# Kernel optimization log

Measured on AMD Instinct MI355X. Metric: run time of the kernel, lower is better.

## Reference

```python
import jax, jax.numpy as jnp
import numpy as np

B, M, S = 4, 1024, 1024
D, H, FF = 1024, 16, 4096
NE, P = 128, 1
HD = D // H
EPS = 1e-5


def _layer_norm(x, g, b):
    mu = x.mean(-1, keepdims=True)
    var = ((x - mu) ** 2).mean(-1, keepdims=True)
    return (x - mu) * jax.lax.rsqrt(var + EPS) * g + b


def _mha(q_in, kv_in, in_w, in_b, out_w, out_b):
    # torch nn.MultiheadAttention: packed in_proj_weight [3D, D], y = x @ W.T + b
    wq, wk, wv = in_w[:D], in_w[D:2 * D], in_w[2 * D:]
    bq, bk, bv = in_b[:D], in_b[D:2 * D], in_b[2 * D:]
    q = (q_in @ wq.T + bq).reshape(q_in.shape[0], q_in.shape[1], H, HD)
    k = (kv_in @ wk.T + bk).reshape(kv_in.shape[0], kv_in.shape[1], H, HD)
    v = (kv_in @ wv.T + bv).reshape(kv_in.shape[0], kv_in.shape[1], H, HD)
    scores = jnp.einsum('bqhd,bkhd->bhqk', q, k) / jnp.sqrt(jnp.float32(HD))
    attn = jax.nn.softmax(scores, axis=-1)
    o = jnp.einsum('bhqk,bkhd->bqhd', attn, v).reshape(q_in.shape[0], q_in.shape[1], D)
    return o @ out_w.T + out_b


def _soft_moe(h, phi, exp_w, exp_b):
    # h: [b, m, FF]; phi: [FF, n, p]
    logits = jnp.einsum('bmd,dnp->bmnp', h, phi)
    dispatch = jax.nn.softmax(logits, axis=1)  # over tokens m
    b, m, n, p = logits.shape
    combine = jax.nn.softmax(logits.reshape(b, m, n * p), axis=-1).reshape(b, m, n, p)
    slots = jnp.einsum('bmd,bmnp->bnpd', h, dispatch)  # [b, n, p, FF]
    y = jnp.einsum('bnpd,ndo->bnpo', slots, exp_w) + exp_b[None, :, None, :]  # [b, n, p, D]
    return jnp.einsum('bnpo,bmnp->bmo', y, combine)


def setup_inputs() -> dict:
    key = jax.random.key(0)
    ks = jax.random.split(key, 16)
    sc = 0.02

    def rn(k, shape):
        return jax.random.normal(k, shape, jnp.float32) * sc

    return {
        'tgt': jax.random.normal(ks[0], (B, M, D), jnp.float32),
        'memory': jax.random.normal(ks[1], (B, S, D), jnp.float32),
        'sa_in_w': rn(ks[2], (3 * D, D)), 'sa_in_b': jnp.zeros((3 * D,), jnp.float32),
        'sa_out_w': rn(ks[3], (D, D)), 'sa_out_b': jnp.zeros((D,), jnp.float32),
        'ca_in_w': rn(ks[4], (3 * D, D)), 'ca_in_b': jnp.zeros((3 * D,), jnp.float32),
        'ca_out_w': rn(ks[5], (D, D)), 'ca_out_b': jnp.zeros((D,), jnp.float32),
        'norm1_g': jnp.ones((D,), jnp.float32), 'norm1_b': jnp.zeros((D,), jnp.float32),
        'norm2_g': jnp.ones((D,), jnp.float32), 'norm2_b': jnp.zeros((D,), jnp.float32),
        'norm3_g': jnp.ones((D,), jnp.float32), 'norm3_b': jnp.zeros((D,), jnp.float32),
        'lin_w': rn(ks[6], (FF, D)), 'lin_b': jnp.zeros((FF,), jnp.float32),
        'phi': rn(ks[7], (FF, NE, P)),
        'exp_w': rn(ks[8], (NE, FF, D)), 'exp_b': jnp.zeros((NE, D), jnp.float32),
    }


def reference(tgt, memory, sa_in_w, sa_in_b, sa_out_w, sa_out_b,
              ca_in_w, ca_in_b, ca_out_w, ca_out_b,
              norm1_g, norm1_b, norm2_g, norm2_b, norm3_g, norm3_b,
              lin_w, lin_b, phi, exp_w, exp_b):
    # post-norm (norm_first=False), dropout=0 (eval)
    x = tgt
    x = _layer_norm(x + _mha(x, x, sa_in_w, sa_in_b, sa_out_w, sa_out_b), norm1_g, norm1_b)
    x = _layer_norm(x + _mha(x, memory, ca_in_w, ca_in_b, ca_out_w, ca_out_b), norm2_g, norm2_b)
    h = jax.nn.relu(x @ lin_w.T + lin_b)  # [B, M, FF]
    ff = _soft_moe(h, phi, exp_w, exp_b)  # [B, M, D]
    x = _layer_norm(x + ff, norm3_g, norm3_b)
    return x
```

## Files before the change

kernel.cpp:

```cpp
#include <hip/hip_runtime.h>
#include <cstdint>
#include <cstddef>

typedef unsigned short u16;
typedef unsigned int   u32;
typedef short bf16x8 __attribute__((ext_vector_type(8)));
typedef float f32x4  __attribute__((ext_vector_type(4)));
typedef u16   u16x8  __attribute__((ext_vector_type(8)));
typedef u16   u16x4  __attribute__((ext_vector_type(4)));
typedef u16   u16x2  __attribute__((ext_vector_type(2)));

constexpr int B_  = 4;
constexpr int M_  = 1024;
constexpr int S_  = 1024;
constexpr int D_  = 1024;
constexpr int H_  = 16;
constexpr int FF_ = 4096;
constexpr int NE_ = 128;

__device__ __forceinline__ u16 f2bf(float f) {
    u32 u = __builtin_bit_cast(u32, f);
    u = (u + 0x7fffu + ((u >> 16) & 1u)) >> 16;
    return (u16)u;
}
__device__ __forceinline__ float bf2f(u16 u) {
    u32 x = ((u32)u) << 16;
    return __builtin_bit_cast(float, x);
}
__device__ __forceinline__ void gload_lds16(const u16* g, u16* l) {
    __builtin_amdgcn_global_load_lds(
        (const __attribute__((address_space(1))) u32*)g,
        (__attribute__((address_space(3))) u32*)l, 16, 0, 0);
}

template<int OUT_BF16, int RELU, int HAS_BIAS, int WRITE_HT>
__global__ __launch_bounds__(256) void gemm64_mfma(
    const u16* __restrict__ A, const u16* __restrict__ W,
    const float* __restrict__ bias, void* __restrict__ Cout,
    u16* __restrict__ HT,
    int K, int N, int lda, int ldw,
    size_t sA, size_t sW, size_t sC)
{
    __shared__ u16 As[2][64 * 32];
    __shared__ u16 Bs[2][128 * 32];
    const int tid = threadIdx.x;
    const int w = tid >> 6, l = tid & 63;
    const int fr = l & 15, g = l >> 4;
    const int bm = blockIdx.y * 64, bn = blockIdx.x * 128;
    const u16* Ab = A + (size_t)blockIdx.z * sA;
    const u16* Wb = W + (size_t)blockIdx.z * sW;

    const int qcol = ((l & 3) ^ ((l >> 3) & 3)) * 8;
    const int srow = w * 16 + (l >> 2);
    const u16* aG  = Ab + (size_t)(bm + srow) * lda + qcol;
    const u16* bG0 = Wb + (size_t)(bn + srow) * ldw + qcol;
    const u16* bG1 = bG0 + (size_t)64 * ldw;
    const int wo = w * 512;

    const int qsw = (g ^ ((fr >> 1) & 3)) * 8;

    f32x4 acc[4][2];
#pragma unroll
    for (int m = 0; m < 4; ++m)
#pragma unroll
        for (int n = 0; n < 2; ++n)
#pragma unroll
            for (int q = 0; q < 4; ++q) acc[m][n][q] = 0.f;

    for (int k0 = 0; k0 < K; k0 += 64) {
        __syncthreads();
        gload_lds16(aG,       &As[0][wo]);
        gload_lds16(bG0,      &Bs[0][wo]);
        gload_lds16(bG1,      &Bs[0][2048 + wo]);
        gload_lds16(aG  + 32, &As[1][wo]);
        gload_lds16(bG0 + 32, &Bs[1][wo]);
        gload_lds16(bG1 + 32, &Bs[1][2048 + wo]);
        aG += 64; bG0 += 64; bG1 += 64;
        __syncthreads();
#pragma unroll
        for (int h = 0; h < 2; ++h) {
            bf16x8 af[4], bf[2];
#pragma unroll
            for (int m = 0; m < 4; ++m)
                af[m] = *(const bf16x8*)&As[h][(m * 16 + fr) * 32 + qsw];
#pragma unroll
            for (int n = 0; n < 2; ++n)
                bf[n] = *(const bf16x8*)&Bs[h][(w * 32 + n * 16 + fr) * 32 + qsw];
#pragma unroll
            for (int m = 0; m < 4; ++m)
#pragma unroll
                for (int n = 0; n < 2; ++n)
                    acc[m][n] = __builtin_amdgcn_mfma_f32_16x16x32_bf16(
                        af[m], bf[n], acc[m][n], 0, 0, 0);
        }
    }

    const int row0 = bm + g * 4;
#pragma unroll
    for (int n = 0; n < 2; ++n) {
        const int col = bn + w * 32 + n * 16 + fr;
        float bv = 0.f;
        if (HAS_BIAS) bv = bias[col];
#pragma unroll
        for (int m = 0; m < 4; ++m) {
            const int rowm = row0 + m * 16;
            u16 o[4];
#pragma unroll
            for (int j = 0; j < 4; ++j) {
                float v = acc[m][n][j] + bv;
                if (RELU) v = fmaxf(v, 0.f);
                const size_t idx = (size_t)blockIdx.z * sC +
                                   (size_t)(rowm + j) * N + col;
                if (OUT_BF16) { o[j] = f2bf(v); ((u16*)Cout)[idx] = o[j]; }
                else          { ((float*)Cout)[idx] = v; }
            }
            if (WRITE_HT) {
                u16x4 pk; pk[0] = o[0]; pk[1] = o[1]; pk[2] = o[2]; pk[3] = o[3];
                *(u16x4*)&HT[(((size_t)(rowm >> 10)) * N + col) * 1024 + (rowm & 1023)] = pk;
            }
        }
    }
}

__global__ __launch_bounds__(256) void flash_attn_kernel(
    const u16* __restrict__ Q, int qs,
    const u16* __restrict__ K, int ks,
    const u16* __restrict__ V, int vs,
    u16* __restrict__ O, int Slen)
{
    __shared__ u16 Ks[2][64][72];
    __shared__ u16 Vt[2][64][72];
    __shared__ u16 Pw[4][16][72];
    const int b = blockIdx.z, hh = blockIdx.y;
    const int m0 = blockIdx.x * 64;
    const int tid = threadIdx.x;
    const int w = tid >> 6, l = tid & 63;
    const int lq = l & 15, g = l >> 4;

    bf16x8 qf[2];
    {
        const u16* qp = Q + ((size_t)b * M_ + m0 + w * 16 + lq) * qs + hh * 64;
        u16x8 v0 = *(const u16x8*)(qp + g * 8);
        u16x8 v1 = *(const u16x8*)(qp + 32 + g * 8);
        u16x8 o0, o1;
#pragma unroll
        for (int i = 0; i < 8; ++i) {
            o0[i] = f2bf(bf2f(v0[i]) * 0.125f);
            o1[i] = f2bf(bf2f(v1[i]) * 0.125f);
        }
        qf[0] = __builtin_bit_cast(bf16x8, o0);
        qf[1] = __builtin_bit_cast(bf16x8, o1);
    }

    f32x4 acc_o[4];
#pragma unroll
    for (int nb = 0; nb < 4; ++nb)
#pragma unroll
        for (int j = 0; j < 4; ++j) acc_o[nb][j] = 0.f;
    float m_run = -1e30f, l_run = 0.f;

    const int kp = tid & 31, dg = tid >> 5;
    const int krow = tid >> 2, kcg = (tid & 3) * 16;

    const int nt = Slen >> 6;
    u16x8 kv0, kv1, va, vb;

#define ATT_LOAD(T_)                                                          \
    {                                                                         \
        const u16* kpp = K + ((size_t)b * Slen + (T_) * 64 + krow) * ks + hh * 64 + kcg; \
        kv0 = *(const u16x8*)kpp;                                             \
        kv1 = *(const u16x8*)(kpp + 8);                                       \
        const u16* vp0 = V + ((size_t)b * Slen + (T_) * 64 + 2 * kp) * vs + hh * 64 + dg * 8; \
        va = *(const u16x8*)vp0;                                              \
        vb = *(const u16x8*)(vp0 + vs);                                       \
    }
#define ATT_WRITE(BUF_)                                                       \
    {                                                                         \
        *(u16x8*)&Ks[BUF_][krow][kcg]     = kv0;                              \
        *(u16x8*)&Ks[BUF_][krow][kcg + 8] = kv1;                              \
        _Pragma("unroll") for (int i = 0; i < 8; ++i) {                       \
            u16x2 pk; pk[0] = va[i]; pk[1] = vb[i];                           \
            *(u16x2*)&Vt[BUF_][dg * 8 + i][2 * kp] = pk;                      \
        }                                                                     \
    }

    ATT_LOAD(0)
    ATT_WRITE(0)
    __syncthreads();

    for (int t = 0; t < nt; ++t) {
        if (t + 1 < nt) ATT_LOAD(t + 1)
        const int cb = t & 1;

        f32x4 s4[4];
#pragma unroll
        for (int mb = 0; mb < 4; ++mb) {
            f32x4 z = {0.f, 0.f, 0.f, 0.f};
            bf16x8 a0 = *(const bf16x8*)&Ks[cb][mb * 16 + lq][g * 8];
            bf16x8 a1 = *(const bf16x8*)&Ks[cb][mb * 16 + lq][32 + g * 8];
            z = __builtin_amdgcn_mfma_f32_16x16x32_bf16(a0, qf[0], z, 0, 0, 0);
            z = __builtin_amdgcn_mfma_f32_16x16x32_bf16(a1, qf[1], z, 0, 0, 0);
            s4[mb] = z;
        }

        float pm = -1e30f;
#pragma unroll
        for (int mb = 0; mb < 4; ++mb)
#pragma unroll
            for (int j = 0; j < 4; ++j) pm = fmaxf(pm, s4[mb][j]);
        pm = fmaxf(pm, __shfl_xor(pm, 16));
        pm = fmaxf(pm, __shfl_xor(pm, 32));

        u16 pbf[4][4];
        float ls = 0.f;
        if (__all(pm - m_run <= 8.f)) {
#pragma unroll
            for (int mb = 0; mb < 4; ++mb)
#pragma unroll
                for (int j = 0; j < 4; ++j) {
                    float p = __expf(s4[mb][j] - m_run);
                    ls += p;
                    pbf[mb][j] = f2bf(p);
                }
            ls += __shfl_xor(ls, 16);
            ls += __shfl_xor(ls, 32);
            l_run += ls;
        } else {
            const float m_new = fmaxf(m_run, pm);
            const float alpha = __expf(m_run - m_new);
#pragma unroll
            for (int mb = 0; mb < 4; ++mb)
#pragma unroll
                for (int j = 0; j < 4; ++j) {
                    float p = __expf(s4[mb][j] - m_new);
                    ls += p;
                    pbf[mb][j] = f2bf(p);
                }
            ls += __shfl_xor(ls, 16);
            ls += __shfl_xor(ls, 32);
            l_run = l_run * alpha + ls;
            m_run = m_new;
            float al[4];
#pragma unroll
            for (int j = 0; j < 4; ++j) al[j] = __shfl(alpha, 4 * g + j);
#pragma unroll
            for (int nb = 0; nb < 4; ++nb)
#pragma unroll
                for (int j = 0; j < 4; ++j) acc_o[nb][j] *= al[j];
        }

#pragma unroll
        for (int mb = 0; mb < 4; ++mb) {
            u16x4 pk;
            pk[0] = pbf[mb][0]; pk[1] = pbf[mb][1];
            pk[2] = pbf[mb][2]; pk[3] = pbf[mb][3];
            *(u16x4*)&Pw[w][lq][mb * 16 + g * 4] = pk;
        }

#pragma unroll
        for (int kc = 0; kc < 2; ++kc) {
            bf16x8 pa = *(const bf16x8*)&Pw[w][lq][kc * 32 + g * 8];
#pragma unroll
            for (int nb = 0; nb < 4; ++nb) {
                bf16x8 bv = *(const bf16x8*)&Vt[cb][nb * 16 + lq][kc * 32 + g * 8];
                acc_o[nb] = __builtin_amdgcn_mfma_f32_16x16x32_bf16(pa, bv, acc_o[nb], 0, 0, 0);
            }
        }

        if (t + 1 < nt) ATT_WRITE((t + 1) & 1)
        __syncthreads();
    }
#undef ATT_LOAD
#undef ATT_WRITE

    float linv[4];
#pragma unroll
    for (int j = 0; j < 4; ++j) linv[j] = 1.f / __shfl(l_run, 4 * g + j);
#pragma unroll
    for (int nb = 0; nb < 4; ++nb)
#pragma unroll
        for (int j = 0; j < 4; ++j) {
            const size_t row = (size_t)b * M_ + m0 + w * 16 + 4 * g + j;
            O[row * D_ + hh * 64 + nb * 16 + lq] = f2bf(acc_o[nb][j] * linv[j]);
        }
}

__global__ __launch_bounds__(256) void cvt_multi_kernel(
    const float* __restrict__ s0, u16* __restrict__ d0,
    const float* __restrict__ s1, u16* __restrict__ d1,
    const float* __restrict__ s2, u16* __restrict__ d2,
    const float* __restrict__ s3, u16* __restrict__ d3,
    const float* __restrict__ s4, u16* __restrict__ d4,
    const float* __restrict__ s5, u16* __restrict__ d5,
    const float* __restrict__ s6, u16* __restrict__ d6)
{
    int blk = blockIdx.x;
    const float* s; u16* d;
    if      (blk < 2048) { s = s0; d = d0; }
    else if (blk < 4096) { s = s1; d = d1; blk -= 2048; }
    else if (blk < 5632) { s = s2; d = d2; blk -= 4096; }
    else if (blk < 6144) { s = s3; d = d3; blk -= 5632; }
    else if (blk < 7680) { s = s4; d = d4; blk -= 6144; }
    else if (blk < 8192) { s = s5; d = d5; blk -= 7680; }
    else                 { s = s6; d = d6; blk -= 8192; }
    const size_t i = ((size_t)blk * 256 + threadIdx.x) * 8;
    float4 a = *(const float4*)(s + i);
    float4 b = *(const float4*)(s + i + 4);
    u16x8 o;
    o[0] = f2bf(a.x); o[1] = f2bf(a.y); o[2] = f2bf(a.z); o[3] = f2bf(a.w);
    o[4] = f2bf(b.x); o[5] = f2bf(b.y); o[6] = f2bf(b.z); o[7] = f2bf(b.w);
    *(u16x8*)(d + i) = o;
}

__global__ __launch_bounds__(256) void transpose_f32_bf16_kernel(
    const float* __restrict__ src, u16* __restrict__ dst, int R, int C,
    size_t sI, size_t sO)
{
    __shared__ u16 t[32][33];
    src += (size_t)blockIdx.z * sI;
    dst += (size_t)blockIdx.z * sO;
    const int c0 = blockIdx.x * 32, r0 = blockIdx.y * 32;
    const int x = threadIdx.x & 31, y = threadIdx.x >> 5;
    for (int i = y; i < 32; i += 8)
        t[i][x] = f2bf(src[(size_t)(r0 + i) * C + c0 + x]);
    __syncthreads();
    for (int i = y; i < 32; i += 8)
        dst[(size_t)(c0 + i) * R + r0 + x] = t[x][i];
}

__global__ __launch_bounds__(256) void resid_ln_kernel(
    const float* __restrict__ X, const float* __restrict__ R,
    const float* __restrict__ g, const float* __restrict__ bt,
    float* __restrict__ Y, u16* __restrict__ Ybf)
{
    __shared__ float s1[4], s2[4];
    const size_t row = blockIdx.x;
    const int tid = threadIdx.x;
    const float4 x4 = *(const float4*)(X + row * 1024 + tid * 4);
    const float4 r4 = *(const float4*)(R + row * 1024 + tid * 4);
    float v[4] = {x4.x + r4.x, x4.y + r4.y, x4.z + r4.z, x4.w + r4.w};
    float s = v[0] + v[1] + v[2] + v[3];
    float q = v[0] * v[0] + v[1] * v[1] + v[2] * v[2] + v[3] * v[3];
#pragma unroll
    for (int off = 32; off; off >>= 1) {
        s += __shfl_xor(s, off);
        q += __shfl_xor(q, off);
    }
    if ((tid & 63) == 0) { s1[tid >> 6] = s; s2[tid >> 6] = q; }
    __syncthreads();
    s = s1[0] + s1[1] + s1[2] + s1[3];
    q = s2[0] + s2[1] + s2[2] + s2[3];
    const float mu = s * (1.f / 1024.f);
    const float var = q * (1.f / 1024.f) - mu * mu;
    const float rinv = rsqrtf(var + 1e-5f);
    const float4 g4 = *(const float4*)(g + tid * 4);
    const float4 b4 = *(const float4*)(bt + tid * 4);
    float o[4];
    o[0] = (v[0] - mu) * rinv * g4.x + b4.x;
    o[1] = (v[1] - mu) * rinv * g4.y + b4.y;
    o[2] = (v[2] - mu) * rinv * g4.z + b4.z;
    o[3] = (v[3] - mu) * rinv * g4.w + b4.w;
    *(float4*)(Y + row * 1024 + tid * 4) = *(float4*)o;
    if (Ybf) {
        u16x4 ob;
        ob[0] = f2bf(o[0]); ob[1] = f2bf(o[1]);
        ob[2] = f2bf(o[2]); ob[3] = f2bf(o[3]);
        *(u16x4*)(Ybf + row * 1024 + tid * 4) = ob;
    }
}

__global__ __launch_bounds__(256) void dispatch_softmax_T_kernel(
    const float* __restrict__ logitsP, u16* __restrict__ dispT)
{
    __shared__ float red[4];
    constexpr size_t CH = (size_t)B_ * M_ * NE_;
    const int n = blockIdx.x, b = blockIdx.y;
    u16* O = dispT + ((size_t)b * NE_ + n) * M_;
    const int tid = threadIdx.x;
    float v[4];
#pragma unroll
    for (int i = 0; i < 4; ++i) {
        const size_t idx = (size_t)(b * M_ + tid + 256 * i) * NE_ + n;
        v[i] = logitsP[idx] + logitsP[CH + idx] + logitsP[2 * CH + idx] + logitsP[3 * CH + idx];
    }
    float mx = fmaxf(fmaxf(v[0], v[1]), fmaxf(v[2], v[3]));
#pragma unroll
    for (int off = 32; off; off >>= 1) mx = fmaxf(mx, __shfl_xor(mx, off));
    if ((tid & 63) == 0) red[tid >> 6] = mx;
    __syncthreads();
    mx = fmaxf(fmaxf(red[0], red[1]), fmaxf(red[2], red[3]));
    __syncthreads();
    float e[4], s = 0.f;
#pragma unroll
    for (int i = 0; i < 4; ++i) { e[i] = __expf(v[i] - mx); s += e[i]; }
#pragma unroll
    for (int off = 32; off; off >>= 1) s += __shfl_xor(s, off);
    if ((tid & 63) == 0) red[tid >> 6] = s;
    __syncthreads();
    s = red[0] + red[1] + red[2] + red[3];
    const float inv = 1.f / s;
#pragma unroll
    for (int i = 0; i < 4; ++i) O[tid + 256 * i] = f2bf(e[i] * inv);
}

__global__ __launch_bounds__(64) void combine_softmax_kernel(
    const float* __restrict__ logitsP, u16* __restrict__ comb)
{
    constexpr size_t CH = (size_t)B_ * M_ * NE_;
    const size_t row = blockIdx.x;
    const int lane = threadIdx.x;
    const size_t i0 = row * NE_ + lane;
    const size_t i1 = i0 + 64;
    float a = logitsP[i0] + logitsP[CH + i0] + logitsP[2 * CH + i0] + logitsP[3 * CH + i0];
    float c = logitsP[i1] + logitsP[CH + i1] + logitsP[2 * CH + i1] + logitsP[3 * CH + i1];
    float mx = fmaxf(a, c);
#pragma unroll
    for (int off = 32; off; off >>= 1) mx = fmaxf(mx, __shfl_xor(mx, off));
    float e0 = __expf(a - mx), e1 = __expf(c - mx);
    float s = e0 + e1;
#pragma unroll
    for (int off = 32; off; off >>= 1) s += __shfl_xor(s, off);
    const float inv = 1.f / s;
    comb[row * NE_ + lane]      = f2bf(e0 * inv);
    comb[row * NE_ + lane + 64] = f2bf(e1 * inv);
}

__global__ __launch_bounds__(256) void expert_partial_kernel(
    const float* __restrict__ slots, const float* __restrict__ exp_w,
    float* __restrict__ part)
{
    __shared__ float sl[4][512];
    const int n = blockIdx.x;
    const int c = blockIdx.y;
    const int f0 = c * 512;
    const int t = threadIdx.x;
    for (int i = t; i < 2048; i += 256) {
        const int b = i >> 9, f = i & 511;
        sl[b][f] = slots[((size_t)b * NE_ + n) * FF_ + f0 + f];
    }
    __syncthreads();
    const int d4 = t * 4;
    const float* wp = exp_w + ((size_t)n * FF_ + f0) * D_ + d4;
    f32x4 acc[4];
#pragma unroll
    for (int b = 0; b < 4; ++b)
#pragma unroll
        for (int j = 0; j < 4; ++j) acc[b][j] = 0.f;
#pragma unroll 4
    for (int f = 0; f < 512; ++f) {
        const float4 w4 = *(const float4*)wp;
        wp += D_;
#pragma unroll
        for (int b = 0; b < 4; ++b) {
            const float s = sl[b][f];
            acc[b][0] = fmaf(s, w4.x, acc[b][0]);
            acc[b][1] = fmaf(s, w4.y, acc[b][1]);
            acc[b][2] = fmaf(s, w4.z, acc[b][2]);
            acc[b][3] = fmaf(s, w4.w, acc[b][3]);
        }
    }
#pragma unroll
    for (int b = 0; b < 4; ++b)
        *(f32x4*)&part[(((size_t)c * 4 + b) * NE_ + n) * D_ + d4] = acc[b];
}

__global__ __launch_bounds__(256) void reduce_yT_kernel(
    const float* __restrict__ part, const float* __restrict__ exp_b,
    u16* __restrict__ yT)
{
    __shared__ float tile[32][33];
    const int d0 = blockIdx.x * 32, n0 = blockIdx.y * 32, b = blockIdx.z;
    const int x = threadIdx.x & 31, y = threadIdx.x >> 5;
    for (int i = y; i < 32; i += 8) {
        const int n = n0 + i;
        float s = exp_b[(size_t)n * D_ + d0 + x];
#pragma unroll
        for (int c = 0; c < 8; ++c)
            s += part[(((size_t)c * 4 + b) * NE_ + n) * D_ + d0 + x];
        tile[i][x] = s;
    }
    __syncthreads();
    for (int i = y; i < 32; i += 8)
        yT[((size_t)b * D_ + d0 + i) * NE_ + n0 + x] = f2bf(tile[x][i]);
}

extern "C" void kernel_launch(void* const* d_in, const int* in_sizes, int n_in,
                              void* d_out, int out_size, void* d_ws, size_t ws_size,
                              hipStream_t stream)
{
    const float* tgt      = (const float*)d_in[0];
    const float* memry    = (const float*)d_in[1];
    const float* sa_in_w  = (const float*)d_in[2];
    const float* sa_in_b  = (const float*)d_in[3];
    const float* sa_out_w = (const float*)d_in[4];
    const float* sa_out_b = (const float*)d_in[5];
    const float* ca_in_w  = (const float*)d_in[6];
    const float* ca_in_b  = (const float*)d_in[7];
    const float* ca_out_w = (const float*)d_in[8];
    const float* ca_out_b = (const float*)d_in[9];
    const float* norm1_g  = (const float*)d_in[10];
    const float* norm1_b  = (const float*)d_in[11];
    const float* norm2_g  = (const float*)d_in[12];
    const float* norm2_b  = (const float*)d_in[13];
    const float* norm3_g  = (const float*)d_in[14];
    const float* norm3_b  = (const float*)d_in[15];
    const float* lin_w    = (const float*)d_in[16];
    const float* lin_b    = (const float*)d_in[17];
    const float* phi      = (const float*)d_in[18];
    const float* exp_w    = (const float*)d_in[19];
    const float* exp_b    = (const float*)d_in[20];

    float* ws = (float*)d_ws;
    u16*   qkv_bf  = (u16*)(ws);
    float* proj    = ws + 6291456;
    float* x1      = ws + 10485760;
    float* x2      = ws + 14680064;
    float* logitsP = ws + 18874368;
    float* part    = ws + 20971520;
    u16*   h_bf    = (u16*)(ws + 25165824);
    u16*   hT_bf   = (u16*)(ws + 33554432);
    u16*   obuf_bf = (u16*)(ws + 41943040);
    u16*   x1_bf   = (u16*)(ws + 44040192);
    u16*   x2_bf   = (u16*)(ws + 46137344);
    u16*   tgt_bf  = (u16*)(ws + 48234496);
    u16*   mem_bf  = (u16*)(ws + 50331648);
    u16*   dispT   = (u16*)(ws + 52428800);
    u16*   comb_bf = (u16*)(ws + 52690944);
    u16*   yT_bf   = (u16*)(ws + 52953088);
    float* slots   = ws + 53215232;
    u16*   w_sa_in = (u16*)(ws + 55312384);
    u16*   w_sa_out= (u16*)(ws + 56885248);
    u16*   w_ca_in = (u16*)(ws + 57409536);
    u16*   w_ca_out= (u16*)(ws + 58982400);
    u16*   w_lin   = (u16*)(ws + 59506688);
    u16*   phiT    = (u16*)(ws + 61603840);

    constexpr size_t CH = (size_t)B_ * M_ * NE_;

    cvt_multi_kernel<<<10240, 256, 0, stream>>>(
        tgt, tgt_bf, memry, mem_bf, sa_in_w, w_sa_in, sa_out_w, w_sa_out,
        ca_in_w, w_ca_in, ca_out_w, w_ca_out, lin_w, w_lin);
    transpose_f32_bf16_kernel<<<dim3(4, 128, 1), 256, 0, stream>>>(phi, phiT, 4096, 128, 0, 0);

    gemm64_mfma<1, 0, 1, 0><<<dim3(24, 64, 1), 256, 0, stream>>>(
        tgt_bf, w_sa_in, sa_in_b, qkv_bf, nullptr, 1024, 3072, 1024, 1024, 0, 0, 0);
    flash_attn_kernel<<<dim3(16, 16, 4), 256, 0, stream>>>(
        qkv_bf, 3072, qkv_bf + 1024, 3072, qkv_bf + 2048, 3072, obuf_bf, S_);
    gemm64_mfma<0, 0, 1, 0><<<dim3(8, 64, 1), 256, 0, stream>>>(
        obuf_bf, w_sa_out, sa_out_b, proj, nullptr, 1024, 1024, 1024, 1024, 0, 0, 0);
    resid_ln_kernel<<<4096, 256, 0, stream>>>(tgt, proj, norm1_g, norm1_b, x1, x1_bf);

    u16* qca_bf = qkv_bf;
    u16* kvca_bf = qkv_bf + (size_t)4096 * 1024;
    gemm64_mfma<1, 0, 1, 0><<<dim3(8, 64, 1), 256, 0, stream>>>(
        x1_bf, w_ca_in, ca_in_b, qca_bf, nullptr, 1024, 1024, 1024, 1024, 0, 0, 0);
    gemm64_mfma<1, 0, 1, 0><<<dim3(16, 64, 1), 256, 0, stream>>>(
        mem_bf, w_ca_in + (size_t)1024 * 1024, ca_in_b + 1024,
        kvca_bf, nullptr, 1024, 2048, 1024, 1024, 0, 0, 0);
    flash_attn_kernel<<<dim3(16, 16, 4), 256, 0, stream>>>(
        qca_bf, 1024, kvca_bf, 2048, kvca_bf + 1024, 2048, obuf_bf, S_);
    gemm64_mfma<0, 0, 1, 0><<<dim3(8, 64, 1), 256, 0, stream>>>(
        obuf_bf, w_ca_out, ca_out_b, proj, nullptr, 1024, 1024, 1024, 1024, 0, 0, 0);
    resid_ln_kernel<<<4096, 256, 0, stream>>>(x1, proj, norm2_g, norm2_b, x2, x2_bf);

    gemm64_mfma<1, 1, 1, 1><<<dim3(32, 64, 1), 256, 0, stream>>>(
        x2_bf, w_lin, lin_b, h_bf, hT_bf, 1024, 4096, 1024, 1024, 0, 0, 0);
    gemm64_mfma<0, 0, 0, 0><<<dim3(1, 64, 4), 256, 0, stream>>>(
        h_bf, phiT, nullptr, logitsP, nullptr, 1024, 128, 4096, 4096,
        1024, 1024, CH);
    dispatch_softmax_T_kernel<<<dim3(NE_, B_), 256, 0, stream>>>(logitsP, dispT);
    combine_softmax_kernel<<<dim3(B_ * M_), 64, 0, stream>>>(logitsP, comb_bf);
    gemm64_mfma<0, 0, 0, 0><<<dim3(32, 2, 4), 256, 0, stream>>>(
        dispT, hT_bf, nullptr, slots, nullptr, 1024, 4096, 1024, 1024,
        (size_t)NE_ * M_, (size_t)FF_ * M_, (size_t)NE_ * FF_);
    expert_partial_kernel<<<dim3(NE_, 8), 256, 0, stream>>>(slots, exp_w, part);
    reduce_yT_kernel<<<dim3(32, 4, 4), 256, 0, stream>>>(part, exp_b, yT_bf);
    gemm64_mfma<0, 0, 0, 0><<<dim3(8, 16, 4), 256, 0, stream>>>(
        comb_bf, yT_bf, nullptr, proj, nullptr, 128, 1024, 128, 128,
        (size_t)M_ * NE_, (size_t)D_ * NE_, (size_t)M_ * D_);
    resid_ln_kernel<<<4096, 256, 0, stream>>>(x2, proj, norm3_g, norm3_b,
                                              (float*)d_out, nullptr);
}
```

Before: 785.5 us.

## Widen flash attention blocks to 128 queries and keep residual path in bf16

Flash attention now runs 512 threads per block covering 128 query rows, so each staged K/V tile is shared by twice as many queries. Only half the threads stage V, and each thread loads one K vector. Separately, the out-projection and MoE-combine GEMMs now write bf16 instead of fp32. The residual+LayerNorm kernels read bf16 inputs and emit only bf16, except the final one, which emits fp32. This cuts global memory traffic and drops the fp32 x1/x2 buffers, at the cost of extra rounding on the residual stream and fewer attention blocks in flight.

```diff
diff --git a/kernel.cpp b/kernel.cpp
--- a/kernel.cpp
+++ b/kernel.cpp
@@ -122,7 +122,7 @@
     }
 }
 
-__global__ __launch_bounds__(256) void flash_attn_kernel(
+__global__ __launch_bounds__(512) void flash_attn_kernel(
     const u16* __restrict__ Q, int qs,
     const u16* __restrict__ K, int ks,
     const u16* __restrict__ V, int vs,
@@ -130,9 +130,9 @@
 {
     __shared__ u16 Ks[2][64][72];
     __shared__ u16 Vt[2][64][72];
-    __shared__ u16 Pw[4][16][72];
+    __shared__ u16 Pw[8][16][72];
     const int b = blockIdx.z, hh = blockIdx.y;
-    const int m0 = blockIdx.x * 64;
+    const int m0 = blockIdx.x * 128;
     const int tid = threadIdx.x;
     const int w = tid >> 6, l = tid & 63;
     const int lq = l & 15, g = l >> 4;
@@ -159,28 +159,31 @@
         for (int j = 0; j < 4; ++j) acc_o[nb][j] = 0.f;
     float m_run = -1e30f, l_run = 0.f;
 
-    const int kp = tid & 31, dg = tid >> 5;
-    const int krow = tid >> 2, kcg = (tid & 3) * 16;
+    const int krow = tid >> 3, kcg = (tid & 7) * 8;
+    const int kp = tid & 31, dg = (tid >> 5) & 7;
+    const int vstage = (tid < 256);
 
     const int nt = Slen >> 6;
-    u16x8 kv0, kv1, va, vb;
+    u16x8 kv0, va, vb;
 
 #define ATT_LOAD(T_)                                                          \
     {                                                                         \
         const u16* kpp = K + ((size_t)b * Slen + (T_) * 64 + krow) * ks + hh * 64 + kcg; \
         kv0 = *(const u16x8*)kpp;                                             \
-        kv1 = *(const u16x8*)(kpp + 8);                                       \
-        const u16* vp0 = V + ((size_t)b * Slen + (T_) * 64 + 2 * kp) * vs + hh * 64 + dg * 8; \
-        va = *(const u16x8*)vp0;                                              \
-        vb = *(const u16x8*)(vp0 + vs);                                       \
+        if (vstage) {                                                         \
+            const u16* vp0 = V + ((size_t)b * Slen + (T_) * 64 + 2 * kp) * vs + hh * 64 + dg * 8; \
+            va = *(const u16x8*)vp0;                                          \
+            vb = *(const u16x8*)(vp0 + vs);                                   \
+        }                                                                     \
     }
 #define ATT_WRITE(BUF_)                                                       \
     {                                                                         \
-        *(u16x8*)&Ks[BUF_][krow][kcg]     = kv0;                              \
-        *(u16x8*)&Ks[BUF_][krow][kcg + 8] = kv1;                              \
-        _Pragma("unroll") for (int i = 0; i < 8; ++i) {                       \
-            u16x2 pk; pk[0] = va[i]; pk[1] = vb[i];                           \
-            *(u16x2*)&Vt[BUF_][dg * 8 + i][2 * kp] = pk;                      \
+        *(u16x8*)&Ks[BUF_][krow][kcg] = kv0;                                  \
+        if (vstage) {                                                         \
+            _Pragma("unroll") for (int i = 0; i < 8; ++i) {                   \
+                u16x2 pk; pk[0] = va[i]; pk[1] = vb[i];                       \
+                *(u16x2*)&Vt[BUF_][dg * 8 + i][2 * kp] = pk;                  \
+            }                                                                 \
         }                                                                     \
     }
 
@@ -328,17 +331,28 @@
         dst[(size_t)(c0 + i) * R + r0 + x] = t[x][i];
 }
 
+template<int X_BF16, int OUT_F32>
 __global__ __launch_bounds__(256) void resid_ln_kernel(
-    const float* __restrict__ X, const float* __restrict__ R,
+    const void* __restrict__ X, const u16* __restrict__ Rb,
     const float* __restrict__ g, const float* __restrict__ bt,
-    float* __restrict__ Y, u16* __restrict__ Ybf)
+    void* __restrict__ Yout)
 {
     __shared__ float s1[4], s2[4];
     const size_t row = blockIdx.x;
     const int tid = threadIdx.x;
-    const float4 x4 = *(const float4*)(X + row * 1024 + tid * 4);
-    const float4 r4 = *(const float4*)(R + row * 1024 + tid * 4);
-    float v[4] = {x4.x + r4.x, x4.y + r4.y, x4.z + r4.z, x4.w + r4.w};
+    float xv[4];
+    if (X_BF16) {
+        u16x4 x4 = *(const u16x4*)((const u16*)X + row * 1024 + tid * 4);
+#pragma unroll
+        for (int i = 0; i < 4; ++i) xv[i] = bf2f(x4[i]);
+    } else {
+        float4 x4 = *(const float4*)((const float*)X + row * 1024 + tid * 4);
+        xv[0] = x4.x; xv[1] = x4.y; xv[2] = x4.z; xv[3] = x4.w;
+    }
+    u16x4 r4 = *(const u16x4*)(Rb + row * 1024 + tid * 4);
+    float v[4];
+#pragma unroll
+    for (int i = 0; i < 4; ++i) v[i] = xv[i] + bf2f(r4[i]);
     float s = v[0] + v[1] + v[2] + v[3];
     float q = v[0] * v[0] + v[1] * v[1] + v[2] * v[2] + v[3] * v[3];
 #pragma unroll
@@ -360,12 +374,13 @@
     o[1] = (v[1] - mu) * rinv * g4.y + b4.y;
     o[2] = (v[2] - mu) * rinv * g4.z + b4.z;
     o[3] = (v[3] - mu) * rinv * g4.w + b4.w;
-    *(float4*)(Y + row * 1024 + tid * 4) = *(float4*)o;
-    if (Ybf) {
+    if (OUT_F32) {
+        *(float4*)((float*)Yout + row * 1024 + tid * 4) = *(float4*)o;
+    } else {
         u16x4 ob;
         ob[0] = f2bf(o[0]); ob[1] = f2bf(o[1]);
         ob[2] = f2bf(o[2]); ob[3] = f2bf(o[3]);
-        *(u16x4*)(Ybf + row * 1024 + tid * 4) = ob;
+        *(u16x4*)((u16*)Yout + row * 1024 + tid * 4) = ob;
     }
 }
 
@@ -512,9 +527,7 @@
 
     float* ws = (float*)d_ws;
     u16*   qkv_bf  = (u16*)(ws);
-    float* proj    = ws + 6291456;
-    float* x1      = ws + 10485760;
-    float* x2      = ws + 14680064;
+    u16*   proj_bf = (u16*)(ws + 6291456);
     float* logitsP = ws + 18874368;
     float* part    = ws + 20971520;
     u16*   h_bf    = (u16*)(ws + 25165824);
@@ -544,11 +557,11 @@
 
     gemm64_mfma<1, 0, 1, 0><<<dim3(24, 64, 1), 256, 0, stream>>>(
         tgt_bf, w_sa_in, sa_in_b, qkv_bf, nullptr, 1024, 3072, 1024, 1024, 0, 0, 0);
-    flash_attn_kernel<<<dim3(16, 16, 4), 256, 0, stream>>>(
+    flash_attn_kernel<<<dim3(8, 16, 4), 512, 0, stream>>>(
         qkv_bf, 3072, qkv_bf + 1024, 3072, qkv_bf + 2048, 3072, obuf_bf, S_);
-    gemm64_mfma<0, 0, 1, 0><<<dim3(8, 64, 1), 256, 0, stream>>>(
-        obuf_bf, w_sa_out, sa_out_b, proj, nullptr, 1024, 1024, 1024, 1024, 0, 0, 0);
-    resid_ln_kernel<<<4096, 256, 0, stream>>>(tgt, proj, norm1_g, norm1_b, x1, x1_bf);
+    gemm64_mfma<1, 0, 1, 0><<<dim3(8, 64, 1), 256, 0, stream>>>(
+        obuf_bf, w_sa_out, sa_out_b, proj_bf, nullptr, 1024, 1024, 1024, 1024, 0, 0, 0);
+    resid_ln_kernel<0, 0><<<4096, 256, 0, stream>>>(tgt, proj_bf, norm1_g, norm1_b, x1_bf);
 
     u16* qca_bf = qkv_bf;
     u16* kvca_bf = qkv_bf + (size_t)4096 * 1024;
@@ -557,11 +570,11 @@
     gemm64_mfma<1, 0, 1, 0><<<dim3(16, 64, 1), 256, 0, stream>>>(
         mem_bf, w_ca_in + (size_t)1024 * 1024, ca_in_b + 1024,
         kvca_bf, nullptr, 1024, 2048, 1024, 1024, 0, 0, 0);
-    flash_attn_kernel<<<dim3(16, 16, 4), 256, 0, stream>>>(
+    flash_attn_kernel<<<dim3(8, 16, 4), 512, 0, stream>>>(
         qca_bf, 1024, kvca_bf, 2048, kvca_bf + 1024, 2048, obuf_bf, S_);
-    gemm64_mfma<0, 0, 1, 0><<<dim3(8, 64, 1), 256, 0, stream>>>(
-        obuf_bf, w_ca_out, ca_out_b, proj, nullptr, 1024, 1024, 1024, 1024, 0, 0, 0);
-    resid_ln_kernel<<<4096, 256, 0, stream>>>(x1, proj, norm2_g, norm2_b, x2, x2_bf);
+    gemm64_mfma<1, 0, 1, 0><<<dim3(8, 64, 1), 256, 0, stream>>>(
+        obuf_bf, w_ca_out, ca_out_b, proj_bf, nullptr, 1024, 1024, 1024, 1024, 0, 0, 0);
+    resid_ln_kernel<1, 0><<<4096, 256, 0, stream>>>(x1_bf, proj_bf, norm2_g, norm2_b, x2_bf);
 
     gemm64_mfma<1, 1, 1, 1><<<dim3(32, 64, 1), 256, 0, stream>>>(
         x2_bf, w_lin, lin_b, h_bf, hT_bf, 1024, 4096, 1024, 1024, 0, 0, 0);
@@ -575,9 +588,9 @@
         (size_t)NE_ * M_, (size_t)FF_ * M_, (size_t)NE_ * FF_);
     expert_partial_kernel<<<dim3(NE_, 8), 256, 0, stream>>>(slots, exp_w, part);
     reduce_yT_kernel<<<dim3(32, 4, 4), 256, 0, stream>>>(part, exp_b, yT_bf);
-    gemm64_mfma<0, 0, 0, 0><<<dim3(8, 16, 4), 256, 0, stream>>>(
-        comb_bf, yT_bf, nullptr, proj, nullptr, 128, 1024, 128, 128,
+    gemm64_mfma<1, 0, 0, 0><<<dim3(8, 16, 4), 256, 0, stream>>>(
+        comb_bf, yT_bf, nullptr, proj_bf, nullptr, 128, 1024, 128, 128,
         (size_t)M_ * NE_, (size_t)D_ * NE_, (size_t)M_ * D_);
-    resid_ln_kernel<<<4096, 256, 0, stream>>>(x2, proj, norm3_g, norm3_b,
-                                              (float*)d_out, nullptr);
-}
+    resid_ln_kernel<1, 1><<<4096, 256, 0, stream>>>(x2_bf, proj_bf, norm3_g, norm3_b,
+                                                    (float*)d_out);
+}
```

New measurement: 748.1 us. 1.05x faster.
